# Optimization experiments

Hardware: AMD Instinct MI355X
Metric: run time of the kernel (lower is better)

## Reference

```python
import jax, jax.numpy as jnp
import numpy as np

CANVAS_W = 1024.0
CANVAS_H = 1024.0
EPS = 1e-8
GOLDEN = 1.618
ALIGN_THRESH = 5.0


def _mse(p, t):
    return jnp.mean((p - t) ** 2)


def _smooth_l1(p, t):
    d = jnp.abs(p - t)
    return jnp.mean(jnp.where(d < 1.0, 0.5 * d * d, d - 0.5))


def setup_inputs() -> dict:
    key = jax.random.key(0)
    k1, k2, k3, k4 = jax.random.split(key, 4)
    B, N, D = 64, 256, 6
    return {
        "predicted_noise": jax.random.normal(k1, (B, N, D), dtype=jnp.float32),
        "target_noise": jax.random.normal(k2, (B, N, D), dtype=jnp.float32),
        "predicted_layout": jax.random.normal(k3, (B, N, D), dtype=jnp.float32),
        "target_layout": jax.random.normal(k4, (B, N, D), dtype=jnp.float32),
        "element_mask": jnp.ones((B, N), dtype=jnp.float32),
    }


def _iou_loss(pred, target):
    # boxes are (x, y, w, h)
    px1, py1 = pred[..., 0], pred[..., 1]
    px2, py2 = px1 + pred[..., 2], py1 + pred[..., 3]
    tx1, ty1 = target[..., 0], target[..., 1]
    tx2, ty2 = tx1 + target[..., 2], ty1 + target[..., 3]
    inter = jnp.maximum(jnp.minimum(px2, tx2) - jnp.maximum(px1, tx1), 0.0) * \
            jnp.maximum(jnp.minimum(py2, ty2) - jnp.maximum(py1, ty1), 0.0)
    pa = pred[..., 2] * pred[..., 3]
    ta = target[..., 2] * target[..., 3]
    iou = inter / (pa + ta - inter + EPS)
    return jnp.mean(1.0 - iou)


def _loss(predicted_noise, target_noise, predicted_layout, target_layout, element_mask):
    B, N, _ = predicted_noise.shape
    mask3 = element_mask[..., None]  # [B,N,1]
    pn = predicted_noise * mask3
    tn = target_noise * mask3
    pl = predicted_layout * mask3
    tl = target_layout * mask3

    npairs = N * (N - 1) / 2.0
    tri = jnp.triu(jnp.ones((N, N), dtype=pl.dtype), k=1)  # i<j pair mask
    pair_valid = element_mask[:, :, None] * element_mask[:, None, :]  # [B,N,N]

    # ---- noise loss (SmoothL1) ----
    noise_loss = _smooth_l1(pn, tn)

    # ---- position loss: MSE + 0.5*IoU ----
    position_loss = _mse(pl[..., :4], tl[..., :4]) + 0.5 * _iou_loss(pl[..., :4], tl[..., :4])

    # ---- layer loss: MSE + 0.3*pairwise ranking BCE ----
    p_layer, t_layer = pl[..., 4], tl[..., 4]
    diff = p_layer[:, None, :] - p_layer[:, :, None]          # [b,i,j] = p_j - p_i
    y = (t_layer[:, :, None] < t_layer[:, None, :]).astype(pl.dtype)
    # BCE(sigmoid(diff), y): -log sigmoid(d)=softplus(-d); torch clamps log terms at 100
    bce = y * jnp.minimum(jax.nn.softplus(-diff), 100.0) + \
          (1.0 - y) * jnp.minimum(jax.nn.softplus(diff), 100.0)
    ranking = jnp.sum(bce * tri) / (B * npairs)
    layer_loss = _mse(p_layer, t_layer) + 0.3 * ranking

    # ---- confidence loss ----
    confidence_loss = _mse(pl[..., 5], tl[..., 5])

    # ---- aesthetic loss ----
    aspect = pl[..., 2] / (pl[..., 3] + EPS)
    golden = jnp.mean(jnp.abs(aspect - GOLDEN))
    areas = pl[..., 2] * pl[..., 3] * element_mask
    size_harm = jnp.mean(jnp.std(areas, axis=1, ddof=1)) / (jnp.mean(areas) + EPS)
    cx = (pl[..., 0] + pl[..., 2] / 2) * element_mask
    cy = (pl[..., 1] + pl[..., 3] / 2) * element_mask
    valid_count = jnp.sum(element_mask, axis=1, keepdims=True)  # [B,1]
    # NOTE: faithful to original broadcasting ([B] / [B,1] -> [B,B])
    ocx = jnp.sum(cx, axis=1) / (valid_count + EPS)
    ocy = jnp.sum(cy, axis=1) / (valid_count + EPS)
    balance = jnp.mean(jnp.abs(ocx - CANVAS_W / 2) / (CANVAS_W / 2) +
                       jnp.abs(ocy - CANVAS_H / 2) / (CANVAS_H / 2))
    aesthetic_loss = 0.1 * golden + 0.2 * size_harm + 0.15 * balance

    # ---- overlap loss (pairwise) ----
    x1, y1, w, h = pl[..., 0], pl[..., 1], pl[..., 2], pl[..., 3]
    x2, y2 = x1 + w, y1 + h
    iw = jnp.maximum(jnp.minimum(x2[:, :, None], x2[:, None, :]) -
                     jnp.maximum(x1[:, :, None], x1[:, None, :]), 0.0)
    ih = jnp.maximum(jnp.minimum(y2[:, :, None], y2[:, None, :]) -
                     jnp.maximum(y1[:, :, None], y1[:, None, :]), 0.0)
    area = w * h
    min_area = jnp.minimum(area[:, :, None], area[:, None, :])
    overlap_ratio = (iw * ih) / (min_area + EPS) * pair_valid
    overlap_loss = jnp.sum(overlap_ratio * tri) / (B * npairs)

    # ---- alignment loss (6 edge types, pairwise) ----
    edges = jnp.stack([x1, x2, y1, y2, x1 + w / 2, y1 + h / 2], axis=0)  # [6,B,N]
    dist = jnp.abs(edges[:, :, :, None] - edges[:, :, None, :])          # [6,B,N,N]
    pen = jnp.where(dist < ALIGN_THRESH, dist / ALIGN_THRESH, 0.0) * pair_valid[None]
    alignment_loss = jnp.sum(pen * tri) / (B * 6.0 * npairs)

    total = (noise_loss + 1.0 * position_loss + 0.5 * layer_loss +
             0.3 * confidence_loss + 0.2 * aesthetic_loss +
             0.8 * overlap_loss + 0.4 * alignment_loss)
    return total


def reference(predicted_noise, target_noise, predicted_layout, target_layout, element_mask):
    return _loss(predicted_noise, target_noise, predicted_layout, target_layout, element_mask)
```

## Files before the change

### kernel.cpp

```cpp
#include <hip/hip_runtime.h>
#include <math.h>

#define NB 64
#define NN 256
#define NPAIRS 32640.0f
#define EPSF 1e-8f

#define PB(q) ((q) * 64)
#define PW(q) (704 + (q) * 512)

__device__ __forceinline__ float block_sum(float v, float* sred) {
    const int tid = threadIdx.x;
    #pragma unroll
    for (int off = 32; off > 0; off >>= 1) v += __shfl_down(v, off, 64);
    __syncthreads();
    if ((tid & 63) == 0) sred[tid >> 6] = v;
    __syncthreads();
    return sred[0] + sred[1] + sred[2] + sred[3];
}

__global__ __launch_bounds__(256) void loss_main(
    const float* __restrict__ pn, const float* __restrict__ tn,
    const float* __restrict__ pl, const float* __restrict__ tl,
    const float* __restrict__ mask, float* __restrict__ ws)
{
    __shared__ float4 sA[NN], sB[NN];
    __shared__ float2 sC[NN];
    __shared__ float sred[4];

    const int b     = blockIdx.x >> 3;
    const int chunk = blockIdx.x & 7;
    const int i     = threadIdx.x;
    const int e     = b * NN + i;
    const float m   = mask[e];

    const float2* pl2 = (const float2*)pl;
    const float2* tl2 = (const float2*)tl;
    const int r2 = e * 3;
    const float2 pla = pl2[r2 + 0], plb = pl2[r2 + 1], plc = pl2[r2 + 2];
    const float2 tlc = tl2[r2 + 2];

    const float p0 = pla.x * m, p1 = pla.y * m,
                p2 = plb.x * m, p3 = plb.y * m,
                p4 = plc.x * m, p5 = plc.y * m;
    const float t4 = tlc.x * m, t5 = tlc.y * m;

    const float x2v = p0 + p2, y2v = p1 + p3;
    const float areav = p2 * p3;
    const float cxe = p0 + 0.5f * p2, cye = p1 + 0.5f * p3;

    sA[i] = make_float4(p0, p1, x2v, y2v);
    sB[i] = make_float4(cxe, cye, areav, p4);
    sC[i] = make_float2(t4, m);
    __syncthreads();

    float rank = 0.f, ovl = 0.f, aln = 0.f;
    const int dd0 = chunk * 16 + 1;
    #pragma unroll 8
    for (int dd = dd0; dd < dd0 + 16; ++dd) {
        int j = (i + dd) & 255;
        if (dd == 128 && i >= 128) continue;
        float4 aj = sA[j];
        float4 bj = sB[j];
        float2 cj = sC[j];
        float pv = m * cj.y;
        float ow = fmaxf(fminf(x2v, aj.z) - fmaxf(p0, aj.x), 0.f);
        float oh = fmaxf(fminf(y2v, aj.w) - fmaxf(p1, aj.y), 0.f);
        ovl += ow * oh / (fminf(areav, bj.z) + EPSF) * pv;
        float pen = 0.f, d;
        d = fabsf(p0  - aj.x); pen += (d < 5.f) ? d : 0.f;
        d = fabsf(x2v - aj.z); pen += (d < 5.f) ? d : 0.f;
        d = fabsf(p1  - aj.y); pen += (d < 5.f) ? d : 0.f;
        d = fabsf(y2v - aj.w); pen += (d < 5.f) ? d : 0.f;
        d = fabsf(cxe - bj.x); pen += (d < 5.f) ? d : 0.f;
        d = fabsf(cye - bj.y); pen += (d < 5.f) ? d : 0.f;
        aln += pen * 0.2f * pv;
        bool ilt = (i < j);
        float dlo = ilt ? (bj.w - p4) : (p4 - bj.w);
        float ylo = (ilt ? (t4 < cj.x) : (cj.x < t4)) ? 1.f : 0.f;
        float sp  = __logf(1.f + __expf(-fabsf(dlo)));
        float sp_pos = sp + fmaxf(dlo, 0.f);
        float sp_neg = sp + fmaxf(-dlo, 0.f);
        rank += ylo * fminf(sp_neg, 100.f) + (1.f - ylo) * fminf(sp_pos, 100.f);
    }

    float s;
    s = block_sum(rank, sred); if (i == 0) ws[PW(0) + blockIdx.x] = s;
    s = block_sum(ovl,  sred); if (i == 0) ws[PW(1) + blockIdx.x] = s;
    s = block_sum(aln,  sred); if (i == 0) ws[PW(2) + blockIdx.x] = s;

    switch (chunk) {
    case 0: {
        const float2* pn2 = (const float2*)pn;
        const float2* tn2 = (const float2*)tn;
        float noise = 0.f;
        #pragma unroll
        for (int k = 0; k < 3; ++k) {
            float2 a = pn2[r2 + k], bb = tn2[r2 + k];
            float d0 = fabsf(a.x * m - bb.x * m);
            float d1 = fabsf(a.y * m - bb.y * m);
            noise += (d0 < 1.f) ? 0.5f * d0 * d0 : d0 - 0.5f;
            noise += (d1 < 1.f) ? 0.5f * d1 * d1 : d1 - 0.5f;
        }
        s = block_sum(noise, sred); if (i == 0) ws[PB(0) + b] = s;
        break; }
    case 1: {
        const float2 tla = tl2[r2 + 0], tlb = tl2[r2 + 1];
        const float t0 = tla.x * m, t1 = tla.y * m,
                    t2 = tlb.x * m, t3 = tlb.y * m;
        float posmse = (p0 - t0) * (p0 - t0) + (p1 - t1) * (p1 - t1)
                     + (p2 - t2) * (p2 - t2) + (p3 - t3) * (p3 - t3);
        const float tx2 = t0 + t2, ty2 = t1 + t3;
        float iw = fmaxf(fminf(x2v, tx2) - fmaxf(p0, t0), 0.f);
        float ih = fmaxf(fminf(y2v, ty2) - fmaxf(p1, t1), 0.f);
        float inter = iw * ih;
        float iouL = 1.f - inter / (areav + t2 * t3 - inter + EPSF);
        s = block_sum(posmse, sred); if (i == 0) ws[PB(1) + b] = s;
        s = block_sum(iouL,   sred); if (i == 0) ws[PB(2) + b] = s;
        break; }
    case 2: {
        float lmse = (p4 - t4) * (p4 - t4);
        float cmse = (p5 - t5) * (p5 - t5);
        s = block_sum(lmse, sred); if (i == 0) ws[PB(3) + b] = s;
        s = block_sum(cmse, sred); if (i == 0) ws[PB(4) + b] = s;
        break; }
    case 3: {
        float golden = fabsf(p2 / (p3 + EPSF) - 1.618f);
        s = block_sum(golden, sred); if (i == 0) ws[PB(5) + b] = s;
        break; }
    case 4: {
        float areaA = areav * m;
        s = block_sum(areaA, sred); if (i == 0) ws[PB(6) + b] = s;
        break; }
    case 5: {
        float areaA = areav * m;
        s = block_sum(areaA * areaA, sred); if (i == 0) ws[PB(7) + b] = s;
        break; }
    case 6: {
        float cxA = cxe * m, cyA = cye * m;
        s = block_sum(cxA, sred); if (i == 0) ws[PB(8) + b] = s;
        s = block_sum(cyA, sred); if (i == 0) ws[PB(9) + b] = s;
        break; }
    default: {
        s = block_sum(m, sred); if (i == 0) ws[PB(10) + b] = s;
        break; }
    }
}

__global__ __launch_bounds__(256) void loss_final(
    const float* __restrict__ ws, float* __restrict__ out)
{
    __shared__ float sred[4];
    __shared__ float bcx[NB], bcy[NB], bvc[NB];
    const int t = threadIdx.x;

    float v_noise = 0.f, v_pos = 0.f, v_iou = 0.f, v_lm = 0.f, v_cf = 0.f,
          v_go = 0.f, v_ar = 0.f, v_std = 0.f;
    if (t < NB) {
        v_noise = ws[PB(0) + t];
        v_pos   = ws[PB(1) + t];
        v_iou   = ws[PB(2) + t];
        v_lm    = ws[PB(3) + t];
        v_cf    = ws[PB(4) + t];
        v_go    = ws[PB(5) + t];
        v_ar    = ws[PB(6) + t];
        float a2 = ws[PB(7) + t];
        float var = (a2 - v_ar * v_ar * (1.f / 256.f)) * (1.f / 255.f);
        v_std = sqrtf(fmaxf(var, 0.f));
        bcx[t] = ws[PB(8) + t];
        bcy[t] = ws[PB(9) + t];
        bvc[t] = ws[PB(10) + t];
    }
    float v_rank = ws[PW(0) + t] + ws[PW(0) + 256 + t];
    float v_ovl  = ws[PW(1) + t] + ws[PW(1) + 256 + t];
    float v_aln  = ws[PW(2) + t] + ws[PW(2) + 256 + t];
    __syncthreads();

    float v_bal = 0.f;
    if (t < NB) {
        float inv = 1.f / (bvc[t] + EPSF);
        for (int j = 0; j < NB; ++j) {
            v_bal += fabsf(bcx[j] * inv - 512.f) * (1.f / 512.f)
                   + fabsf(bcy[j] * inv - 512.f) * (1.f / 512.f);
        }
    }

    float S_noise = block_sum(v_noise, sred);
    float S_pos   = block_sum(v_pos,   sred);
    float S_iou   = block_sum(v_iou,   sred);
    float S_lm    = block_sum(v_lm,    sred);
    float S_cf    = block_sum(v_cf,    sred);
    float S_go    = block_sum(v_go,    sred);
    float S_ar    = block_sum(v_ar,    sred);
    float S_std   = block_sum(v_std,   sred);
    float S_bal   = block_sum(v_bal,   sred);
    float S_rank  = block_sum(v_rank,  sred);
    float S_ovl   = block_sum(v_ovl,   sred);
    float S_aln   = block_sum(v_aln,   sred);

    if (t == 0) {
        const float BN = 64.f * 256.f;
        float noise_loss = S_noise / (BN * 6.f);
        float position   = S_pos / (BN * 4.f) + 0.5f * (S_iou / BN);
        float layer      = S_lm / BN + 0.3f * (S_rank / (64.f * NPAIRS));
        float conf       = S_cf / BN;
        float golden     = S_go / BN;
        float size_harm  = (S_std / 64.f) / (S_ar / BN + EPSF);
        float balance    = S_bal / 4096.f;
        float aes        = 0.1f * golden + 0.2f * size_harm + 0.15f * balance;
        float ovl        = S_ovl / (64.f * NPAIRS);
        float aln        = S_aln / (64.f * 6.f * NPAIRS);
        out[0] = noise_loss + position + 0.5f * layer + 0.3f * conf
               + 0.2f * aes + 0.8f * ovl + 0.4f * aln;
    }
}

extern "C" void kernel_launch(void* const* d_in, const int* in_sizes, int n_in,
                              void* d_out, int out_size, void* d_ws, size_t ws_size,
                              hipStream_t stream) {
    const float* pn   = (const float*)d_in[0];
    const float* tn   = (const float*)d_in[1];
    const float* pl   = (const float*)d_in[2];
    const float* tl   = (const float*)d_in[3];
    const float* mask = (const float*)d_in[4];
    float* ws  = (float*)d_ws;
    float* out = (float*)d_out;
    hipLaunchKernelGGL(loss_main, dim3(512), dim3(256), 0, stream,
                       pn, tn, pl, tl, mask, ws);
    hipLaunchKernelGGL(loss_final, dim3(1), dim3(256), 0, stream, ws, out);
}
```

Baseline: 74.89 us.

## Fuse final reduction into main kernel using per-block release flags

Merges the two launches into one. Each block publishes a magic flag with a release store to workspace once its partial sums are written. Block 0 then spins with acquire loads until all 512 flags are set and performs the final reduction itself. This removes the second kernel launch and its dependency gap. The flags are never cleared, so on repeated calls block 0 can see stale flags from an earlier run and read partial sums before they are rewritten.

```diff
diff --git a/kernel.cpp b/kernel.cpp
--- a/kernel.cpp
+++ b/kernel.cpp
@@ -5,9 +5,11 @@
 #define NN 256
 #define NPAIRS 32640.0f
 #define EPSF 1e-8f
+#define MAGIC 0x5CA1AB1Eu
 
 #define PB(q) ((q) * 64)
 #define PW(q) (704 + (q) * 512)
+#define FLAGS_OFF 2240
 
 __device__ __forceinline__ float block_sum(float v, float* sred) {
     const int tid = threadIdx.x;
@@ -19,14 +21,16 @@
     return sred[0] + sred[1] + sred[2] + sred[3];
 }
 
-__global__ __launch_bounds__(256) void loss_main(
+__global__ __launch_bounds__(256) void loss_fused(
     const float* __restrict__ pn, const float* __restrict__ tn,
     const float* __restrict__ pl, const float* __restrict__ tl,
-    const float* __restrict__ mask, float* __restrict__ ws)
+    const float* __restrict__ mask, float* __restrict__ ws,
+    float* __restrict__ out)
 {
     __shared__ float4 sA[NN], sB[NN];
     __shared__ float2 sC[NN];
     __shared__ float sred[4];
+    __shared__ float bcx[NB], bcy[NB], bvc[NB];
 
     const int b     = blockIdx.x >> 3;
     const int chunk = blockIdx.x & 7;
@@ -145,15 +149,27 @@
         s = block_sum(m, sred); if (i == 0) ws[PB(10) + b] = s;
         break; }
     }
-}
-
-__global__ __launch_bounds__(256) void loss_final(
-    const float* __restrict__ ws, float* __restrict__ out)
-{
-    __shared__ float sred[4];
-    __shared__ float bcx[NB], bcy[NB], bvc[NB];
-    const int t = threadIdx.x;
-
+
+    unsigned int* flags = (unsigned int*)(ws + FLAGS_OFF);
+    if (i == 0) {
+        __hip_atomic_store(&flags[blockIdx.x], MAGIC,
+                           __ATOMIC_RELEASE, __HIP_MEMORY_SCOPE_AGENT);
+    }
+    if (blockIdx.x != 0) return;
+
+    {
+        bool f1 = false, f2 = false;
+        while (!(f1 && f2)) {
+            if (!f1) f1 = (__hip_atomic_load(&flags[i],
+                            __ATOMIC_ACQUIRE, __HIP_MEMORY_SCOPE_AGENT) == MAGIC);
+            if (!f2) f2 = (__hip_atomic_load(&flags[256 + i],
+                            __ATOMIC_ACQUIRE, __HIP_MEMORY_SCOPE_AGENT) == MAGIC);
+            if (!(f1 && f2)) __builtin_amdgcn_s_sleep(8);
+        }
+    }
+    __syncthreads();
+
+    const int t = i;
     float v_noise = 0.f, v_pos = 0.f, v_iou = 0.f, v_lm = 0.f, v_cf = 0.f,
           v_go = 0.f, v_ar = 0.f, v_std = 0.f;
     if (t < NB) {
@@ -225,7 +241,6 @@
     const float* mask = (const float*)d_in[4];
     float* ws  = (float*)d_ws;
     float* out = (float*)d_out;
-    hipLaunchKernelGGL(loss_main, dim3(512), dim3(256), 0, stream,
-                       pn, tn, pl, tl, mask, ws);
-    hipLaunchKernelGGL(loss_final, dim3(1), dim3(256), 0, stream, ws, out);
+    hipLaunchKernelGGL(loss_fused, dim3(512), dim3(256), 0, stream,
+                       pn, tn, pl, tl, mask, ws, out);
 }
```

Result: slower. 80.34 us (+7.3%).
